# Kernel tuning notes

Hardware: AMD Instinct MI355X
Metric: run time of the kernel (lower is better)

The kernel has to match this reference:

```python
import jax, jax.numpy as jnp
import numpy as np

B, T, C = 512, 2048, 32

def setup_inputs() -> dict:
    key = jax.random.key(0)
    k1, k2, k3, k4 = jax.random.split(key, 4)
    target_predict = jax.random.normal(k1, (B, T, C), dtype=jnp.float32)
    trans = jax.random.uniform(k2, (C, C), dtype=jnp.float32)
    # labels in [0, C]; label value C is the padded class dropped by [:, :, :-1]
    target_true = jax.random.randint(k3, (B, T), 0, C + 1, dtype=jnp.int64)
    lens = jax.random.randint(k4, (B,), 0, T, dtype=jnp.int64)
    return {"target_predict": target_predict, "trans": trans,
            "target_true": target_true, "lens": lens}

def reference(target_predict, trans, target_true, lens):
    dt = target_predict.dtype
    c = trans.shape[0]
    # one_hot with depth C+1, drop last column (pad class) -> [B, T, C]
    oh = jax.nn.one_hot(target_true, c + 1, dtype=dt)[:, :, :-1]
    # emission score of the true path
    sum_h = jnp.sum(target_predict * oh, axis=(1, 2))  # [B]
    # g_mtx[b,t,i,j] = sum_k trans[i,k]*pre[b,t,k]*fut[b,t,j]; summed over t,i,j
    pre, fut = oh[:, :-1, :], oh[:, 1:, :]
    sum_g = jnp.einsum('ik,btk,btj->b', trans, pre, fut)  # [B]
    # forward-algorithm partition via scan; carry Z_col [B, C]
    lens_f = lens.astype(dt)
    Z_col0 = target_predict[:, 0, :]
    emis = jnp.swapaxes(target_predict[:, 1:, :], 0, 1)  # [T-1, B, C]
    steps = jnp.arange(1, target_predict.shape[1], dtype=dt)
    def step(Z_col, xs):
        e_t, t = xs
        valid = (lens_f >= t).astype(dt)  # [B]
        # Z_t[b,p,q] = Z_col[b,p] + (e_t[b,q] + trans[p,q]) * mask[b]
        Zt = Z_col[:, :, None] + (e_t[:, None, :] + trans) * valid[:, None, None]
        Z_sum = jax.scipy.special.logsumexp(Zt, axis=2)  # [B, C]
        Z_col_new = jnp.where(valid[:, None] > 0, Z_sum, Z_col)
        return Z_col_new, None
    Z_col, _ = jax.lax.scan(step, Z_col0, (emis, steps))
    # final Z_t is Z_col broadcast along last axis -> sum over [1,2] = C * sum(Z_col)
    sum_Z = jnp.asarray(c, dt) * jnp.sum(Z_col, axis=1)  # [B]
    return jnp.mean(sum_Z - sum_h - sum_g)
```

## Files before the change

### kernel.cpp

```cpp
#include <hip/hip_runtime.h>

#define BDIM 512
#define TDIM 2048
#define CDIM 32
#define BLOCK 256
#define CHUNKS (TDIM / BLOCK)
#define NBLK (BDIM * CHUNKS)


__global__ void crf_prep(const float* __restrict__ trans, float* __restrict__ ws) {
    int i = threadIdx.x;
    float* colsum = ws;
    float* E = ws + 32;
    E[i] = __expf(trans[i]);
    if (i < CDIM) {
        float s = 0.f;
        #pragma unroll
        for (int r = 0; r < CDIM; ++r) s += trans[r * CDIM + i];
        colsum[i] = s;
    }
}

__global__ __launch_bounds__(BLOCK) void crf_main(
        const float* __restrict__ P, const int* __restrict__ TT,
        const int* __restrict__ LEN, const float* __restrict__ ws,
        float* __restrict__ partials) {
    const float* colsum = ws;
    const float* E = ws + 32;

    const int blk = blockIdx.x;
    const int b = blk >> 3;
    const int chunk = blk & 7;
    const int t = chunk * BLOCK + threadIdx.x;
    const int len = LEN[b];
    const long rowbase = ((long)b * TDIM + t) * CDIM;

    const int tt = TT[b * TDIM + t];
    const int tt2 = (t < TDIM - 1) ? TT[b * TDIM + t + 1] : CDIM;

    float h = 0.f, g = 0.f, z = 0.f;
    if (tt < CDIM) {
        h = P[rowbase + tt];
        if (tt2 < CDIM) g = colsum[tt];
    }

    const bool heavy = (t >= 1 && t <= len);
    if (heavy || t == 0) {
        const float4* row4 = reinterpret_cast<const float4*>(P + rowbase);
        float p[CDIM];
        #pragma unroll
        for (int q = 0; q < 8; ++q) {
            float4 v = row4[q];
            p[q * 4 + 0] = v.x; p[q * 4 + 1] = v.y;
            p[q * 4 + 2] = v.z; p[q * 4 + 3] = v.w;
        }
        if (t == 0) {
            float s = 0.f;
            #pragma unroll
            for (int y = 0; y < CDIM; ++y) s += p[y];
            z = s;
        } else {
            float ep[CDIM];
            #pragma unroll
            for (int y = 0; y < CDIM; ++y) ep[y] = __expf(p[y]);
            float R2 = 0.f;
            #pragma unroll
            for (int x = 0; x < CDIM; x += 4) {
                float a0 = 0.f, a1 = 0.f, a2 = 0.f, a3 = 0.f;
                #pragma unroll
                for (int y = 0; y < CDIM; ++y) {
                    a0 = fmaf(ep[y], E[(x + 0) * CDIM + y], a0);
                    a1 = fmaf(ep[y], E[(x + 1) * CDIM + y], a1);
                    a2 = fmaf(ep[y], E[(x + 2) * CDIM + y], a2);
                    a3 = fmaf(ep[y], E[(x + 3) * CDIM + y], a3);
                }
                R2 += __log2f(a0) + __log2f(a1) + __log2f(a2) + __log2f(a3);
            }
            z = R2 * 0.6931471805599453f;
        }
    }

    float v = 32.f * z - h - g;
    #pragma unroll
    for (int off = 32; off; off >>= 1) v += __shfl_down(v, off);
    __shared__ float red[BLOCK / 64];
    if ((threadIdx.x & 63) == 0) red[threadIdx.x >> 6] = v;
    __syncthreads();
    if (threadIdx.x == 0)
        partials[blk] = red[0] + red[1] + red[2] + red[3];
}

__global__ void crf_finish(const float* __restrict__ partials, float* __restrict__ out) {
    double s = 0.0;
    for (int i = threadIdx.x; i < NBLK; i += 256) s += (double)partials[i];
    #pragma unroll
    for (int off = 32; off; off >>= 1) s += __shfl_down(s, off);
    __shared__ double red[4];
    if ((threadIdx.x & 63) == 0) red[threadIdx.x >> 6] = s;
    __syncthreads();
    if (threadIdx.x == 0) out[0] = (float)((red[0] + red[1] + red[2] + red[3]) / (double)BDIM);
}

extern "C" void kernel_launch(void* const* d_in, const int* in_sizes, int n_in,
                              void* d_out, int out_size, void* d_ws, size_t ws_size,
                              hipStream_t stream) {
    const float* P     = (const float*)d_in[0];
    const float* trans = (const float*)d_in[1];
    const int*   TT    = (const int*)d_in[2];
    const int*   LEN   = (const int*)d_in[3];
    float* out = (float*)d_out;
    float* ws  = (float*)d_ws;
    float* partials = ws + 2048;

    hipLaunchKernelGGL(crf_prep,   dim3(1),    dim3(1024), 0, stream, trans, ws);
    hipLaunchKernelGGL(crf_main,   dim3(NBLK), dim3(BLOCK), 0, stream, P, TT, LEN, ws, partials);
    hipLaunchKernelGGL(crf_finish, dim3(1),    dim3(256),  0, stream, partials, out);
}
```

Before: 209.7 us.

## Compute per-step exp-sum matvec with bf16 MFMA and fold prep into main kernel

Replaces the per-thread 32x32 scalar FMA matvec over exp(emissions) and exp(trans) with bf16 MFMA 32x32x16 instructions. Each wave stages its 64 rows of exp(emission) into shared memory as bf16 and multiplies them against exp(trans) held in registers. The separate prep kernel is removed: every block recomputes exp(trans) and the column sums into shared memory itself. This cuts FP32 ALU work and one launch, but rounding the operands to bf16 loses precision inside the logsumexp, and each block now repeats the trans setup.

```diff
diff --git a/kernel.cpp b/kernel.cpp
--- a/kernel.cpp
+++ b/kernel.cpp
@@ -1,4 +1,5 @@
 #include <hip/hip_runtime.h>
+#include <stdint.h>
 
 #define BDIM 512
 #define TDIM 2048
@@ -7,86 +8,130 @@
 #define CHUNKS (TDIM / BLOCK)
 #define NBLK (BDIM * CHUNKS)
 
+using bf16x8 = __attribute__((ext_vector_type(8))) short;
+using f32x16 = __attribute__((ext_vector_type(16))) float;
+using f32x4  = __attribute__((ext_vector_type(4))) float;
 
-__global__ void crf_prep(const float* __restrict__ trans, float* __restrict__ ws) {
-    int i = threadIdx.x;
-    float* colsum = ws;
-    float* E = ws + 32;
-    E[i] = __expf(trans[i]);
-    if (i < CDIM) {
-        float s = 0.f;
-        #pragma unroll
-        for (int r = 0; r < CDIM; ++r) s += trans[r * CDIM + i];
-        colsum[i] = s;
-    }
+__device__ inline unsigned short f2bf(float f) {
+    uint32_t u = __builtin_bit_cast(uint32_t, f);
+    u += 0x7fff + ((u >> 16) & 1);
+    return (unsigned short)(u >> 16);
 }
+
 
 __global__ __launch_bounds__(BLOCK) void crf_main(
         const float* __restrict__ P, const int* __restrict__ TT,
-        const int* __restrict__ LEN, const float* __restrict__ ws,
+        const int* __restrict__ LEN, const float* __restrict__ trans,
         float* __restrict__ partials) {
-    const float* colsum = ws;
-    const float* E = ws + 32;
+    __shared__ unsigned short sEb[CDIM * CDIM];
+    __shared__ float sCol[CDIM];
+    __shared__ unsigned short epBuf[4 * 4 * 64 * 8];
 
-    const int blk = blockIdx.x;
-    const int b = blk >> 3;
+    const int tid  = threadIdx.x;
+    const int lane = tid & 63;
+    const int wid  = tid >> 6;
+
+    #pragma unroll
+    for (int q = 0; q < 4; ++q) {
+        int i = q * BLOCK + tid;
+        sEb[i] = f2bf(__expf(trans[i]));
+    }
+    if (tid < CDIM) {
+        float s = 0.f;
+        #pragma unroll
+        for (int r = 0; r < CDIM; ++r) s += trans[r * CDIM + tid];
+        sCol[tid] = s;
+    }
+    __syncthreads();
+
+    bf16x8 bB0, bB1;
+    {
+        const int n  = lane & 31;
+        const int kh = (lane >> 5) * 8;
+        bB0 = *reinterpret_cast<const bf16x8*>(&sEb[n * CDIM + 0  + kh]);
+        bB1 = *reinterpret_cast<const bf16x8*>(&sEb[n * CDIM + 16 + kh]);
+    }
+
+    const int blk   = blockIdx.x;
+    const int b     = blk >> 3;
     const int chunk = blk & 7;
-    const int t = chunk * BLOCK + threadIdx.x;
-    const int len = LEN[b];
+    const int t     = chunk * BLOCK + tid;
+    const int len   = LEN[b];
     const long rowbase = ((long)b * TDIM + t) * CDIM;
 
-    const int tt = TT[b * TDIM + t];
+    const int tt  = TT[b * TDIM + t];
     const int tt2 = (t < TDIM - 1) ? TT[b * TDIM + t + 1] : CDIM;
 
-    float h = 0.f, g = 0.f, z = 0.f;
+    float h = 0.f, g = 0.f;
     if (tt < CDIM) {
         h = P[rowbase + tt];
-        if (tt2 < CDIM) g = colsum[tt];
+        if (tt2 < CDIM) g = sCol[tt];
     }
 
-    const bool heavy = (t >= 1 && t <= len);
-    if (heavy || t == 0) {
-        const float4* row4 = reinterpret_cast<const float4*>(P + rowbase);
+    float zpart = 0.f;
+    const int tbase = chunk * BLOCK + wid * 64;
+
+    if (tbase <= len) {
+        const bool heavy = (t >= 1) && (t <= len);
         float p[CDIM];
-        #pragma unroll
-        for (int q = 0; q < 8; ++q) {
-            float4 v = row4[q];
-            p[q * 4 + 0] = v.x; p[q * 4 + 1] = v.y;
-            p[q * 4 + 2] = v.z; p[q * 4 + 3] = v.w;
+        if (heavy || t == 0) {
+            const f32x4* row4 = reinterpret_cast<const f32x4*>(P + rowbase);
+            #pragma unroll
+            for (int q = 0; q < 8; ++q) {
+                f32x4 v = row4[q];
+                p[4*q+0] = v[0]; p[4*q+1] = v[1]; p[4*q+2] = v[2]; p[4*q+3] = v[3];
+            }
+        } else {
+            #pragma unroll
+            for (int y = 0; y < CDIM; ++y) p[y] = 0.f;
         }
         if (t == 0) {
             float s = 0.f;
             #pragma unroll
             for (int y = 0; y < CDIM; ++y) s += p[y];
-            z = s;
-        } else {
-            float ep[CDIM];
+            zpart += 32.f * s;
+        }
+
+        unsigned short* epW = epBuf + wid * (4 * 64 * 8);
+        #pragma unroll
+        for (int c = 0; c < 4; ++c) {
+            union { bf16x8 v; unsigned short u[8]; } pk;
             #pragma unroll
-            for (int y = 0; y < CDIM; ++y) ep[y] = __expf(p[y]);
-            float R2 = 0.f;
+            for (int j = 0; j < 8; ++j) {
+                float e = heavy ? __expf(p[c * 8 + j]) : 0.f;
+                pk.u[j] = f2bf(e);
+            }
+            *reinterpret_cast<bf16x8*>(&epW[(c * 64 + lane) * 8]) = pk.v;
+        }
+
+        float zlog = 0.f;
+        const int chi = lane >> 5;
+        #pragma unroll
+        for (int T = 0; T < 2; ++T) {
+            const int m = T * 32 + (lane & 31);
+            bf16x8 a0 = *reinterpret_cast<const bf16x8*>(&epW[((0 + chi) * 64 + m) * 8]);
+            bf16x8 a1 = *reinterpret_cast<const bf16x8*>(&epW[((2 + chi) * 64 + m) * 8]);
+            f32x16 acc = {};
+            acc = __builtin_amdgcn_mfma_f32_32x32x16_bf16(a0, bB0, acc, 0, 0, 0);
+            acc = __builtin_amdgcn_mfma_f32_32x32x16_bf16(a1, bB1, acc, 0, 0, 0);
             #pragma unroll
-            for (int x = 0; x < CDIM; x += 4) {
-                float a0 = 0.f, a1 = 0.f, a2 = 0.f, a3 = 0.f;
-                #pragma unroll
-                for (int y = 0; y < CDIM; ++y) {
-                    a0 = fmaf(ep[y], E[(x + 0) * CDIM + y], a0);
-                    a1 = fmaf(ep[y], E[(x + 1) * CDIM + y], a1);
-                    a2 = fmaf(ep[y], E[(x + 2) * CDIM + y], a2);
-                    a3 = fmaf(ep[y], E[(x + 3) * CDIM + y], a3);
-                }
-                R2 += __log2f(a0) + __log2f(a1) + __log2f(a2) + __log2f(a3);
+            for (int r = 0; r < 16; ++r) {
+                const int row  = (r & 3) + 8 * (r >> 2) + 4 * chi + T * 32;
+                const int trow = tbase + row;
+                const bool valid = (trow >= 1) && (trow <= len);
+                zlog += valid ? __log2f(acc[r]) : 0.f;
             }
-            z = R2 * 0.6931471805599453f;
         }
+        zpart += 32.f * 0.6931471805599453f * zlog;
     }
 
-    float v = 32.f * z - h - g;
+    float v = zpart - h - g;
     #pragma unroll
     for (int off = 32; off; off >>= 1) v += __shfl_down(v, off);
     __shared__ float red[BLOCK / 64];
-    if ((threadIdx.x & 63) == 0) red[threadIdx.x >> 6] = v;
+    if (lane == 0) red[wid] = v;
     __syncthreads();
-    if (threadIdx.x == 0)
+    if (tid == 0)
         partials[blk] = red[0] + red[1] + red[2] + red[3];
 }
 
@@ -112,7 +157,6 @@
     float* ws  = (float*)d_ws;
     float* partials = ws + 2048;
 
-    hipLaunchKernelGGL(crf_prep,   dim3(1),    dim3(1024), 0, stream, trans, ws);
-    hipLaunchKernelGGL(crf_main,   dim3(NBLK), dim3(BLOCK), 0, stream, P, TT, LEN, ws, partials);
-    hipLaunchKernelGGL(crf_finish, dim3(1),    dim3(256),  0, stream, partials, out);
+    hipLaunchKernelGGL(crf_main,   dim3(NBLK), dim3(BLOCK), 0, stream, P, TT, LEN, trans, partials);
+    hipLaunchKernelGGL(crf_finish, dim3(1),    dim3(256),   0, stream, partials, out);
 }
```

Result: faster. 204.4 us (-2.5%).
